# Optimization experiments

Hardware: AMD Instinct MI355X
Metric: run time of the kernel (lower is better)

The kernel has to match this reference:

```python
import jax, jax.numpy as jnp
import numpy as np
from jax import lax

HID = 896          # hidden_size
HALF = HID // 2    # 448
BINS = 256         # 2 ** (bits/2), bits=16
B, T = 16, 2048


def setup_inputs() -> dict:
    key = jax.random.key(0)
    ks = jax.random.split(key, 16)
    rn = lambda k, shape, s: (jax.random.normal(k, shape, jnp.float32) * s)
    inp = {
        'conditional': jax.random.normal(ks[0], (B, T, 3, HID), jnp.float32),
        'input_signal': jax.random.randint(ks[1], (B, T, 2), 0, BINS, jnp.int32),
        'target_coarse': jax.random.randint(ks[2], (B, T, 1), 0, BINS, jnp.int32),
        # project_coarse_input: Linear(2, 3*half, bias=False)
        'Wc': rn(ks[3], (2, 3 * HALF), 0.5),
        # project_fine_input: Linear(3, 3*half, bias=False)
        'Wf': rn(ks[4], (3, 3 * HALF), 0.5),
        # stripped GRU hidden-to-hidden weights/biases (input projection is rnn_input itself)
        'W_hh': rn(ks[5], (HID, 3 * HID), 0.02),
        'b_ih': jnp.zeros((3 * HID,), jnp.float32),
        'b_hh': jnp.zeros((3 * HID,), jnp.float32),
        # to_bins_coarse: Linear(half, half) + ReLU + Linear(half, bins)
        'W1c': rn(ks[6], (HALF, HALF), 0.05), 'b1c': jnp.zeros((HALF,), jnp.float32),
        'W2c': rn(ks[7], (HALF, BINS), 0.05), 'b2c': jnp.zeros((BINS,), jnp.float32),
        # to_bins_fine
        'W1f': rn(ks[8], (HALF, HALF), 0.05), 'b1f': jnp.zeros((HALF,), jnp.float32),
        'W2f': rn(ks[9], (HALF, BINS), 0.05), 'b2f': jnp.zeros((BINS,), jnp.float32),
    }
    return inp


def _scale(x):
    # [0, BINS-1] -> [-1, 1]
    return x.astype(jnp.float32) / ((BINS - 1) / 2.0) - 1.0


def reference(conditional, input_signal, target_coarse, Wc, Wf, W_hh, b_ih, b_hh,
              W1c, b1c, W2c, b2c, W1f, b1f, W2f, b2f):
    sig = _scale(input_signal)          # [B, T, 2]
    tc = _scale(target_coarse)          # [B, T, 1]

    coarse_proj = (sig @ Wc).reshape(B, T, 3, HALF)
    fine_proj = (jnp.concatenate([sig, tc], axis=2) @ Wf).reshape(B, T, 3, HALF)
    # concat along feature halves -> [B, T, 3, HID], add conditional, flatten gates
    rnn_input = jnp.concatenate([coarse_proj, fine_proj], axis=3) + conditional
    rnn_input = rnn_input.reshape(B, T, 3 * HID) + b_ih
    xs = rnn_input.transpose(1, 0, 2)   # [T, B, 3*HID]

    def step(h, x_t):
        gh = h @ W_hh + b_hh                      # [B, 3*HID]
        xr, xz, xn = jnp.split(x_t, 3, axis=-1)
        hr, hz, hn = jnp.split(gh, 3, axis=-1)
        r = jax.nn.sigmoid(xr + hr)
        z = jax.nn.sigmoid(xz + hz)
        n = jnp.tanh(xn + r * hn)
        h_new = (1.0 - z) * n + z * h
        return h_new, h_new

    h0 = jnp.zeros((B, HID), jnp.float32)
    last_hidden, hidden_states = lax.scan(step, h0, xs)   # [T, B, HID]
    hidden_states = hidden_states.transpose(1, 0, 2)      # [B, T, HID]

    hidden_coarse = hidden_states[..., :HALF]
    # NOTE: original code applies to_bins_fine to hidden_coarse as well (faithful).
    out_coarse = jax.nn.relu(hidden_coarse @ W1c + b1c) @ W2c + b2c
    out_fine = jax.nn.relu(hidden_coarse @ W1f + b1f) @ W2f + b2f
    return out_coarse, out_fine, last_hidden
```

## Files before the change

### kernel.cpp

```cpp
#include <hip/hip_runtime.h>
#include <hip/hip_cooperative_groups.h>

namespace cg = cooperative_groups;

#define BB 16
#define TT 2048
#define HIDN 896
#define HALFN 448
#define NBINS 256
#define NWG 224
#define NTHR 64
#define SROW 904
#define WSTR 904

typedef __attribute__((ext_vector_type(8))) short short8;
typedef __attribute__((ext_vector_type(4))) float f32x4;

__device__ __forceinline__ unsigned short f2bf(float x) {
    unsigned int u = __float_as_uint(x);
    unsigned int r = u + 0x7FFFu + ((u >> 16) & 1u);
    return (unsigned short)(r >> 16);
}

__global__ __launch_bounds__(NTHR, 1)
void scan_kernel(const float* __restrict__ cond,
                 const int*   __restrict__ sig,
                 const int*   __restrict__ tcrs,
                 const float* __restrict__ Wc,
                 const float* __restrict__ Wf,
                 const float* __restrict__ Whh,
                 const float* __restrict__ b_ih,
                 const float* __restrict__ b_hh,
                 unsigned long long* __restrict__ hx,
                 int* __restrict__ slots,
                 unsigned short* __restrict__ hc_out,
                 float* __restrict__ lasth)
{
    __shared__ unsigned short sW[16 * WSTR];
    __shared__ unsigned short sH[16 * SROW];

    const int tid  = threadIdx.x;
    const int wg   = blockIdx.x;
    const int col0 = wg * 4;

    for (int idx = tid; idx < 16 * HIDN; idx += NTHR) {
        int j2 = idx & 15, k = idx >> 4;
        unsigned short wv = 0;
        if (j2 < 12)
            wv = f2bf(Whh[(size_t)k * 2688 + (j2 >> 2) * HIDN + col0 + (j2 & 3)]);
        sW[j2 * WSTR + k] = wv;
    }
    for (int idx = tid; idx < (16 * SROW) / 2; idx += NTHR)
        ((unsigned*)sH)[idx] = 0;
    if (tid == 0)
        __hip_atomic_store(&slots[wg], 0, __ATOMIC_RELAXED, __HIP_MEMORY_SCOPE_AGENT);

    const int l  = tid;
    const int jj = l & 15;
    const int hi = l >> 4;
    const bool xrole = jj < 12;
    const int gate = (jj >> 2) & 3;
    const int cc   = jj & 3;
    const int col  = col0 + cc;

    float wp0 = 0.f, wp1 = 0.f, wp2 = 0.f, bi = 0.f, bh = 0.f;
    if (xrole) {
        if (col < HALFN) {
            wp0 = Wc[gate * HALFN + col];
            wp1 = Wc[1344 + gate * HALFN + col];
        } else {
            int ck = col - HALFN;
            wp0 = Wf[gate * HALFN + ck];
            wp1 = Wf[1344 + gate * HALFN + ck];
            wp2 = Wf[2688 + gate * HALFN + ck];
        }
        bi = b_ih[gate * HIDN + col];
        bh = b_hh[gate * HIDN + col];
    }
    float hp[4] = {0.f, 0.f, 0.f, 0.f};

    __syncthreads();
    cg::this_grid().sync();

    const float inv = 1.f / 127.5f;
    const unsigned long long* s64 = (const unsigned long long*)slots;
    const int srcr = (l & 48) | cc;
    const int srcz = (l & 48) | 4 | cc;

#define WAITS(s) { bool ok_;                                                   \
    for (;;) {                                                                 \
        ok_ = true;                                                            \
        if (l < 28) {                                                          \
            unsigned long long a_ = __hip_atomic_load(&s64[28*(s) + l],        \
                __ATOMIC_RELAXED, __HIP_MEMORY_SCOPE_AGENT);                   \
            ok_ = ((int)(a_ & 0xffffffffu) >= t) & ((int)(a_ >> 32) >= t);     \
        }                                                                      \
        if (__all(ok_)) break;                                                 \
        __builtin_amdgcn_s_sleep(1);                                           \
    }                                                                          \
    asm volatile("" ::: "memory"); }

#define LOADS(s, V) _Pragma("unroll")                                          \
    for (int i_ = 0; i_ < 14; ++i_)                                            \
        V[i_] = __hip_atomic_load(&hb[(size_t)((56*(s)) + hi*14 + i_)*16 + jj],\
            __ATOMIC_RELAXED, __HIP_MEMORY_SCOPE_AGENT);

#define STAGES(s, V) _Pragma("unroll")                                         \
    for (int i_ = 0; i_ < 14; ++i_)                                            \
        *(unsigned long long*)&sH[jj * SROW + ((56*(s)) + hi*14 + i_)*4] = V[i_];

#define MFMAS(s) _Pragma("unroll")                                             \
    for (int q_ = 0; q_ < 7; ++q_) {                                           \
        int ks_ = (s)*7 + q_;                                                  \
        short8 av_ = *(const short8*)&sH[jj * SROW + hi * 8 + ks_ * 32];       \
        short8 bv_ = *(const short8*)&sW[jj * WSTR + hi * 8 + ks_ * 32];       \
        ch[(7*(s) + q_) & 3] =                                                 \
            __builtin_amdgcn_mfma_f32_16x16x32_bf16(av_, bv_, ch[(7*(s)+q_)&3],\
                                                    0, 0, 0);                  \
    }

    for (int t = 0; t < TT; ++t) {
        float xc[4], sg0[4], sg1[4], sg2[4];
        if (xrole) {
            #pragma unroll
            for (int r = 0; r < 4; ++r) {
                int b = hi * 4 + r;
                size_t bt = (size_t)b * TT + t;
                xc[r]  = cond[(bt * 3 + gate) * HIDN + col];
                sg0[r] = (float)sig[bt * 2 + 0] * inv - 1.f;
                sg1[r] = (float)sig[bt * 2 + 1] * inv - 1.f;
                sg2[r] = (float)tcrs[bt] * inv - 1.f;
            }
        } else {
            xc[0]=xc[1]=xc[2]=xc[3]=0.f;
            sg0[0]=sg0[1]=sg0[2]=sg0[3]=0.f;
            sg1[0]=sg1[1]=sg1[2]=sg1[3]=0.f;
            sg2[0]=sg2[1]=sg2[2]=sg2[3]=0.f;
        }

        f32x4 ch[4] = {};
        if (t > 0) {
            const unsigned long long* hb = hx + (size_t)(t & 1) * 3584;
            unsigned long long va[14], vb[14];
            WAITS(0); LOADS(0, va);
            WAITS(1); LOADS(1, vb);
            STAGES(0, va); MFMAS(0);
            WAITS(2); LOADS(2, va);
            STAGES(1, vb); MFMAS(1);
            WAITS(3); LOADS(3, vb);
            STAGES(2, va); MFMAS(2);
            STAGES(3, vb); MFMAS(3);
        } else {
            MFMAS(0); MFMAS(1); MFMAS(2); MFMAS(3);
        }

        f32x4 acc = (ch[0] + ch[1]) + (ch[2] + ch[3]);

        float xv[4], sigv[4];
        #pragma unroll
        for (int r = 0; r < 4; ++r) {
            xv[r]   = xc[r] + bi + sg0[r]*wp0 + sg1[r]*wp1 + sg2[r]*wp2;
            sigv[r] = 1.f / (1.f + __expf(-(xv[r] + acc[r] + bh)));
        }
        float rr[4], zz[4];
        #pragma unroll
        for (int r = 0; r < 4; ++r) {
            rr[r] = __shfl(sigv[r], srcr);
            zz[r] = __shfl(sigv[r], srcz);
        }
        unsigned short hbits[4] = {0, 0, 0, 0};
        if (jj >= 8 && jj < 12) {
            #pragma unroll
            for (int r = 0; r < 4; ++r) {
                float a2v = xv[r] + rr[r] * (acc[r] + bh);
                float e = __expf(-2.f * a2v);
                float n = (1.f - e) / (1.f + e);
                float hn = (1.f - zz[r]) * n + zz[r] * hp[r];
                hp[r] = hn;
                hbits[r] = f2bf(hn);
                if (t == TT - 1)
                    lasth[(size_t)(hi * 4 + r) * HIDN + col] = hn;
            }
        }
        unsigned pp32[4];
        unsigned long long hv64[4];
        #pragma unroll
        for (int r = 0; r < 4; ++r) {
            int o1 = __shfl_xor((int)(unsigned)hbits[r], 1);
            unsigned p = ((unsigned)hbits[r] & 0xffffu) | ((unsigned)o1 << 16);
            pp32[r] = p;
            int o2 = __shfl_xor((int)p, 2);
            hv64[r] = (unsigned long long)p | ((unsigned long long)(unsigned)o2 << 32);
        }
        unsigned long long* hd = hx + (size_t)((t + 1) & 1) * 3584;
        if (jj == 8) {
            #pragma unroll
            for (int r = 0; r < 4; ++r)
                __hip_atomic_store(&hd[wg * 16 + hi * 4 + r], hv64[r],
                                   __ATOMIC_RELAXED, __HIP_MEMORY_SCOPE_AGENT);
        }
        asm volatile("s_waitcnt vmcnt(0)" ::: "memory");
        if (tid == 0)
            __hip_atomic_store(&slots[wg], t + 1, __ATOMIC_RELAXED, __HIP_MEMORY_SCOPE_AGENT);

        if (wg < 112 && jj >= 8 && jj < 12 && !(jj & 1)) {
            unsigned* hc32 = (unsigned*)hc_out;
            #pragma unroll
            for (int r = 0; r < 4; ++r)
                hc32[((size_t)(hi * 4 + r) * TT + t) * 224 + wg * 2 + ((jj - 8) >> 1)] = pp32[r];
        }
    }
#undef WAITS
#undef LOADS
#undef STAGES
#undef MFMAS
}

template<int RELU_BF16>
__global__ __launch_bounds__(256)
void head_gemm(const unsigned short* __restrict__ A,
               const float* __restrict__ Bw,
               const float* __restrict__ bias,
               unsigned short* __restrict__ Cb,
               float* __restrict__ Cf,
               int N)
{
    const int K = 448;
    __shared__ float As[32][68];
    __shared__ float Bs[32][68];
    const int tid = threadIdx.x;
    const int tx = tid & 15;
    const int ty = tid >> 4;
    const int bm = blockIdx.x * 64;
    const int bn = blockIdx.y * 64;

    float acc[4][4] = {};

    for (int k0 = 0; k0 < K; k0 += 32) {
        #pragma unroll
        for (int it = 0; it < 2; ++it) {
            int idx = tid + it * 256;
            int m   = idx >> 3;
            int k4  = idx & 7;
            ushort4 av = *(const ushort4*)(A + (size_t)(bm + m) * K + k0 + k4 * 4);
            As[k4 * 4 + 0][m] = __uint_as_float((unsigned)av.x << 16);
            As[k4 * 4 + 1][m] = __uint_as_float((unsigned)av.y << 16);
            As[k4 * 4 + 2][m] = __uint_as_float((unsigned)av.z << 16);
            As[k4 * 4 + 3][m] = __uint_as_float((unsigned)av.w << 16);
        }
        #pragma unroll
        for (int it = 0; it < 2; ++it) {
            int idx = tid + it * 256;
            int k   = idx >> 4;
            int n4  = idx & 15;
            *(float4*)&Bs[k][n4 * 4] =
                *(const float4*)(Bw + (size_t)(k0 + k) * N + bn + n4 * 4);
        }
        __syncthreads();
        #pragma unroll
        for (int k = 0; k < 32; ++k) {
            float4 a4 = *(float4*)&As[k][ty * 4];
            float4 b4 = *(float4*)&Bs[k][tx * 4];
            float ar[4] = {a4.x, a4.y, a4.z, a4.w};
            float br[4] = {b4.x, b4.y, b4.z, b4.w};
            #pragma unroll
            for (int i = 0; i < 4; ++i)
                #pragma unroll
                for (int j = 0; j < 4; ++j)
                    acc[i][j] = fmaf(ar[i], br[j], acc[i][j]);
        }
        __syncthreads();
    }

    float4 bsv = *(const float4*)(bias + bn + tx * 4);
    float bb[4] = {bsv.x, bsv.y, bsv.z, bsv.w};
    #pragma unroll
    for (int i = 0; i < 4; ++i) {
        int row = bm + ty * 4 + i;
        float v[4];
        #pragma unroll
        for (int j = 0; j < 4; ++j) v[j] = acc[i][j] + bb[j];
        if (RELU_BF16) {
            ushort4 o;
            o.x = f2bf(fmaxf(v[0], 0.f));
            o.y = f2bf(fmaxf(v[1], 0.f));
            o.z = f2bf(fmaxf(v[2], 0.f));
            o.w = f2bf(fmaxf(v[3], 0.f));
            *(ushort4*)(Cb + (size_t)row * N + bn + tx * 4) = o;
        } else {
            float4 o = make_float4(v[0], v[1], v[2], v[3]);
            *(float4*)(Cf + (size_t)row * N + bn + tx * 4) = o;
        }
    }
}

extern "C" void kernel_launch(void* const* d_in, const int* in_sizes, int n_in,
                              void* d_out, int out_size, void* d_ws, size_t ws_size,
                              hipStream_t stream)
{
    const float* cond = (const float*)d_in[0];
    const int*   sig  = (const int*)d_in[1];
    const int*   tcrs = (const int*)d_in[2];
    const float* Wc   = (const float*)d_in[3];
    const float* Wf   = (const float*)d_in[4];
    const float* Whh  = (const float*)d_in[5];
    const float* bih  = (const float*)d_in[6];
    const float* bhh  = (const float*)d_in[7];
    const float* W1c  = (const float*)d_in[8];
    const float* b1c  = (const float*)d_in[9];
    const float* W2c  = (const float*)d_in[10];
    const float* b2c  = (const float*)d_in[11];
    const float* W1f  = (const float*)d_in[12];
    const float* b1f  = (const float*)d_in[13];
    const float* W2f  = (const float*)d_in[14];
    const float* b2f  = (const float*)d_in[15];

    char* ws = (char*)d_ws;
    int* slots               = (int*)ws;
    unsigned long long* hx   = (unsigned long long*)(ws + 4096);
    unsigned short* hc       = (unsigned short*)(ws + 65536);
    unsigned short* hid1     = (unsigned short*)(ws + 65536 + 29360128);

    float* outc  = (float*)d_out;
    float* outf  = outc + (size_t)BB * TT * NBINS;
    float* lasth = outc + 2 * (size_t)BB * TT * NBINS;

    void* args[] = {(void*)&cond, (void*)&sig, (void*)&tcrs, (void*)&Wc, (void*)&Wf,
                    (void*)&Whh, (void*)&bih, (void*)&bhh,
                    (void*)&hx, (void*)&slots, (void*)&hc, (void*)&lasth};
    hipLaunchCooperativeKernel((void*)scan_kernel, dim3(NWG), dim3(NTHR),
                               args, 0, stream);

    dim3 blk(256);
    head_gemm<1><<<dim3(512, 7), blk, 0, stream>>>(hc,   W1c, b1c, hid1, nullptr, 448);
    head_gemm<0><<<dim3(512, 4), blk, 0, stream>>>(hid1, W2c, b2c, nullptr, outc, 256);
    head_gemm<1><<<dim3(512, 7), blk, 0, stream>>>(hc,   W1f, b1f, hid1, nullptr, 448);
    head_gemm<0><<<dim3(512, 4), blk, 0, stream>>>(hid1, W2f, b2f, nullptr, outf, 256);
}
```

Before: 9.196 ms.

## Halve scan workgroups, widen per-WG columns, load hidden state directly into MFMA operands

The persistent GRU scan now uses 112 workgroups, each owning 8 hidden columns (r/z and n gates split across two MFMA tiles), instead of 224 groups with 4 columns. The LDS staging of the hidden state is removed: each lane loads its MFMA A operand straight from global memory. Per-workgroup ready flags are padded to separate cache lines and waited on individually. The aim is to cut cross-workgroup synchronisation fan-in and the LDS round-trip on the serial critical path, in exchange for more MFMA and gate work per workgroup per step.

```diff
diff --git a/kernel.cpp b/kernel.cpp
--- a/kernel.cpp
+++ b/kernel.cpp
@@ -8,13 +8,13 @@
 #define HIDN 896
 #define HALFN 448
 #define NBINS 256
-#define NWG 224
+#define NWG 112
 #define NTHR 64
-#define SROW 904
 #define WSTR 904
 
 typedef __attribute__((ext_vector_type(8))) short short8;
 typedef __attribute__((ext_vector_type(4))) float f32x4;
+typedef __attribute__((ext_vector_type(2))) unsigned long long ull2;
 
 __device__ __forceinline__ unsigned short f2bf(float x) {
     unsigned int u = __float_as_uint(x);
@@ -36,183 +36,180 @@
                  unsigned short* __restrict__ hc_out,
                  float* __restrict__ lasth)
 {
-    __shared__ unsigned short sW[16 * WSTR];
-    __shared__ unsigned short sH[16 * SROW];
+    __shared__ unsigned short sW[32 * WSTR];
 
     const int tid  = threadIdx.x;
     const int wg   = blockIdx.x;
-    const int col0 = wg * 4;
-
-    for (int idx = tid; idx < 16 * HIDN; idx += NTHR) {
-        int j2 = idx & 15, k = idx >> 4;
+    const int col0 = wg * 8;
+
+    for (int idx = tid; idx < 32 * HIDN; idx += NTHR) {
+        int j2 = idx & 31, k = idx >> 5;
         unsigned short wv = 0;
-        if (j2 < 12)
-            wv = f2bf(Whh[(size_t)k * 2688 + (j2 >> 2) * HIDN + col0 + (j2 & 3)]);
+        if (j2 < 16)
+            wv = f2bf(Whh[(size_t)k * 2688 + (j2 >> 3) * HIDN + col0 + (j2 & 7)]);
+        else if (j2 < 24)
+            wv = f2bf(Whh[(size_t)k * 2688 + 2 * HIDN + col0 + (j2 & 7)]);
         sW[j2 * WSTR + k] = wv;
     }
-    for (int idx = tid; idx < (16 * SROW) / 2; idx += NTHR)
-        ((unsigned*)sH)[idx] = 0;
     if (tid == 0)
-        __hip_atomic_store(&slots[wg], 0, __ATOMIC_RELAXED, __HIP_MEMORY_SCOPE_AGENT);
+        __hip_atomic_store(&slots[wg * 16], 0, __ATOMIC_RELAXED, __HIP_MEMORY_SCOPE_AGENT);
 
     const int l  = tid;
-    const int jj = l & 15;
+    const int q  = l & 15;
     const int hi = l >> 4;
-    const bool xrole = jj < 12;
-    const int gate = (jj >> 2) & 3;
-    const int cc   = jj & 3;
-    const int col  = col0 + cc;
-
-    float wp0 = 0.f, wp1 = 0.f, wp2 = 0.f, bi = 0.f, bh = 0.f;
-    if (xrole) {
-        if (col < HALFN) {
-            wp0 = Wc[gate * HALFN + col];
-            wp1 = Wc[1344 + gate * HALFN + col];
-        } else {
-            int ck = col - HALFN;
-            wp0 = Wf[gate * HALFN + ck];
-            wp1 = Wf[1344 + gate * HALFN + ck];
-            wp2 = Wf[2688 + gate * HALFN + ck];
-        }
-        bi = b_ih[gate * HIDN + col];
-        bh = b_hh[gate * HIDN + col];
-    }
+    const int gA   = q >> 3;
+    const int colA = col0 + (q & 7);
+
+    float wpA0, wpA1, wpA2, wpB0, wpB1, wpB2;
+    if (colA < HALFN) {
+        wpA0 = Wc[gA * HALFN + colA];
+        wpA1 = Wc[1344 + gA * HALFN + colA];
+        wpA2 = 0.f;
+        wpB0 = Wc[2 * HALFN + colA];
+        wpB1 = Wc[1344 + 2 * HALFN + colA];
+        wpB2 = 0.f;
+    } else {
+        int ck = colA - HALFN;
+        wpA0 = Wf[gA * HALFN + ck];
+        wpA1 = Wf[1344 + gA * HALFN + ck];
+        wpA2 = Wf[2688 + gA * HALFN + ck];
+        wpB0 = Wf[2 * HALFN + ck];
+        wpB1 = Wf[1344 + 2 * HALFN + ck];
+        wpB2 = Wf[2688 + 2 * HALFN + ck];
+    }
+    const float biA = b_ih[gA * HIDN + colA];
+    const float bhA = b_hh[gA * HIDN + colA];
+    const float biB = b_ih[2 * HIDN + colA];
+    const float bhB = b_hh[2 * HIDN + colA];
+
     float hp[4] = {0.f, 0.f, 0.f, 0.f};
 
     __syncthreads();
     cg::this_grid().sync();
 
     const float inv = 1.f / 127.5f;
-    const unsigned long long* s64 = (const unsigned long long*)slots;
-    const int srcr = (l & 48) | cc;
-    const int srcz = (l & 48) | 4 | cc;
+    const int zsrc = (l & 48) | 8 | (q & 7);
 
 #define WAITS(s) { bool ok_;                                                   \
     for (;;) {                                                                 \
         ok_ = true;                                                            \
         if (l < 28) {                                                          \
-            unsigned long long a_ = __hip_atomic_load(&s64[28*(s) + l],        \
+            int a_ = __hip_atomic_load(&slots[((s)*28 + l) * 16],              \
                 __ATOMIC_RELAXED, __HIP_MEMORY_SCOPE_AGENT);                   \
-            ok_ = ((int)(a_ & 0xffffffffu) >= t) & ((int)(a_ >> 32) >= t);     \
+            ok_ = (a_ >= t);                                                   \
         }                                                                      \
         if (__all(ok_)) break;                                                 \
         __builtin_amdgcn_s_sleep(1);                                           \
     }                                                                          \
     asm volatile("" ::: "memory"); }
 
-#define LOADS(s, V) _Pragma("unroll")                                          \
-    for (int i_ = 0; i_ < 14; ++i_)                                            \
-        V[i_] = __hip_atomic_load(&hb[(size_t)((56*(s)) + hi*14 + i_)*16 + jj],\
-            __ATOMIC_RELAXED, __HIP_MEMORY_SCOPE_AGENT);
-
-#define STAGES(s, V) _Pragma("unroll")                                         \
-    for (int i_ = 0; i_ < 14; ++i_)                                            \
-        *(unsigned long long*)&sH[jj * SROW + ((56*(s)) + hi*14 + i_)*4] = V[i_];
-
-#define MFMAS(s) _Pragma("unroll")                                             \
-    for (int q_ = 0; q_ < 7; ++q_) {                                           \
-        int ks_ = (s)*7 + q_;                                                  \
-        short8 av_ = *(const short8*)&sH[jj * SROW + hi * 8 + ks_ * 32];       \
-        short8 bv_ = *(const short8*)&sW[jj * WSTR + hi * 8 + ks_ * 32];       \
-        ch[(7*(s) + q_) & 3] =                                                 \
-            __builtin_amdgcn_mfma_f32_16x16x32_bf16(av_, bv_, ch[(7*(s)+q_)&3],\
-                                                    0, 0, 0);                  \
+#define LOADF(s, V) _Pragma("unroll")                                          \
+    for (int i_ = 0; i_ < 7; ++i_) {                                           \
+        _Pragma("unroll")                                                      \
+        for (int h_ = 0; h_ < 2; ++h_)                                         \
+            V[2*i_ + h_] = __hip_atomic_load(                                  \
+                &hb[(size_t)(4 * ((s)*7 + i_) + hi) * 32 + h_ * 16 + q],       \
+                __ATOMIC_RELAXED, __HIP_MEMORY_SCOPE_AGENT);                   \
+    }
+
+#define MFMAS(s, V) _Pragma("unroll")                                          \
+    for (int i_ = 0; i_ < 7; ++i_) {                                           \
+        ull2 tv_; tv_.x = V[2*i_]; tv_.y = V[2*i_ + 1];                        \
+        short8 av_ = __builtin_bit_cast(short8, tv_);                          \
+        int ks_ = (s)*7 + i_;                                                  \
+        short8 b1_ = *(const short8*)&sW[q * WSTR + hi * 8 + ks_ * 32];        \
+        chA[ks_ & 3] = __builtin_amdgcn_mfma_f32_16x16x32_bf16(                \
+            av_, b1_, chA[ks_ & 3], 0, 0, 0);                                  \
+        short8 b2_ = *(const short8*)&sW[(16 + q) * WSTR + hi * 8 + ks_ * 32]; \
+        chB[ks_ & 3] = __builtin_amdgcn_mfma_f32_16x16x32_bf16(                \
+            av_, b2_, chB[ks_ & 3], 0, 0, 0);                                  \
     }
 
     for (int t = 0; t < TT; ++t) {
-        float xc[4], sg0[4], sg1[4], sg2[4];
-        if (xrole) {
-            #pragma unroll
-            for (int r = 0; r < 4; ++r) {
-                int b = hi * 4 + r;
-                size_t bt = (size_t)b * TT + t;
-                xc[r]  = cond[(bt * 3 + gate) * HIDN + col];
-                sg0[r] = (float)sig[bt * 2 + 0] * inv - 1.f;
-                sg1[r] = (float)sig[bt * 2 + 1] * inv - 1.f;
-                sg2[r] = (float)tcrs[bt] * inv - 1.f;
-            }
-        } else {
-            xc[0]=xc[1]=xc[2]=xc[3]=0.f;
-            sg0[0]=sg0[1]=sg0[2]=sg0[3]=0.f;
-            sg1[0]=sg1[1]=sg1[2]=sg1[3]=0.f;
-            sg2[0]=sg2[1]=sg2[2]=sg2[3]=0.f;
-        }
-
-        f32x4 ch[4] = {};
+        float xcA[4], xcB[4], sg0[4], sg1[4], sg2[4];
+        #pragma unroll
+        for (int r = 0; r < 4; ++r) {
+            int b = hi * 4 + r;
+            size_t bt = (size_t)b * TT + t;
+            xcA[r] = cond[(bt * 3 + gA) * HIDN + colA];
+            xcB[r] = cond[(bt * 3 + 2) * HIDN + colA];
+            sg0[r] = (float)sig[bt * 2 + 0] * inv - 1.f;
+            sg1[r] = (float)sig[bt * 2 + 1] * inv - 1.f;
+            sg2[r] = (float)tcrs[bt] * inv - 1.f;
+        }
+
+        f32x4 chA[4] = {}, chB[4] = {};
         if (t > 0) {
             const unsigned long long* hb = hx + (size_t)(t & 1) * 3584;
             unsigned long long va[14], vb[14];
-            WAITS(0); LOADS(0, va);
-            WAITS(1); LOADS(1, vb);
-            STAGES(0, va); MFMAS(0);
-            WAITS(2); LOADS(2, va);
-            STAGES(1, vb); MFMAS(1);
-            WAITS(3); LOADS(3, vb);
-            STAGES(2, va); MFMAS(2);
-            STAGES(3, vb); MFMAS(3);
-        } else {
-            MFMAS(0); MFMAS(1); MFMAS(2); MFMAS(3);
-        }
-
-        f32x4 acc = (ch[0] + ch[1]) + (ch[2] + ch[3]);
-
-        float xv[4], sigv[4];
+            WAITS(0); LOADF(0, va);
+            WAITS(1); LOADF(1, vb);
+            MFMAS(0, va);
+            WAITS(2); LOADF(2, va);
+            MFMAS(1, vb);
+            WAITS(3); LOADF(3, vb);
+            MFMAS(2, va);
+            MFMAS(3, vb);
+        }
+        f32x4 aA = (chA[0] + chA[1]) + (chA[2] + chA[3]);
+        f32x4 aB = (chB[0] + chB[1]) + (chB[2] + chB[3]);
+
+        float xvA[4], xvB[4], sigA[4];
         #pragma unroll
         for (int r = 0; r < 4; ++r) {
-            xv[r]   = xc[r] + bi + sg0[r]*wp0 + sg1[r]*wp1 + sg2[r]*wp2;
-            sigv[r] = 1.f / (1.f + __expf(-(xv[r] + acc[r] + bh)));
-        }
-        float rr[4], zz[4];
+            xvA[r] = xcA[r] + biA + sg0[r]*wpA0 + sg1[r]*wpA1 + sg2[r]*wpA2;
+            xvB[r] = xcB[r] + biB + sg0[r]*wpB0 + sg1[r]*wpB1 + sg2[r]*wpB2;
+            sigA[r] = 1.f / (1.f + __expf(-(xvA[r] + aA[r] + bhA)));
+        }
+        float hnv[4];
+        unsigned short hbits[4] = {0, 0, 0, 0};
         #pragma unroll
         for (int r = 0; r < 4; ++r) {
-            rr[r] = __shfl(sigv[r], srcr);
-            zz[r] = __shfl(sigv[r], srcz);
-        }
-        unsigned short hbits[4] = {0, 0, 0, 0};
-        if (jj >= 8 && jj < 12) {
+            float zz = __shfl(sigA[r], zsrc);
+            float a2v = xvB[r] + sigA[r] * (aB[r] + bhB);
+            float e = __expf(-2.f * a2v);
+            float n = (1.f - e) / (1.f + e);
+            float hn = (1.f - zz) * n + zz * hp[r];
+            hnv[r] = hn;
+            if (q < 8) { hp[r] = hn; hbits[r] = f2bf(hn); }
+        }
+        if (t == TT - 1 && q < 8) {
             #pragma unroll
-            for (int r = 0; r < 4; ++r) {
-                float a2v = xv[r] + rr[r] * (acc[r] + bh);
-                float e = __expf(-2.f * a2v);
-                float n = (1.f - e) / (1.f + e);
-                float hn = (1.f - zz[r]) * n + zz[r] * hp[r];
-                hp[r] = hn;
-                hbits[r] = f2bf(hn);
-                if (t == TT - 1)
-                    lasth[(size_t)(hi * 4 + r) * HIDN + col] = hn;
-            }
-        }
-        unsigned pp32[4];
+            for (int r = 0; r < 4; ++r)
+                lasth[(size_t)(hi * 4 + r) * HIDN + colA] = hnv[r];
+        }
+
+        unsigned p32[4];
         unsigned long long hv64[4];
         #pragma unroll
         for (int r = 0; r < 4; ++r) {
             int o1 = __shfl_xor((int)(unsigned)hbits[r], 1);
-            unsigned p = ((unsigned)hbits[r] & 0xffffu) | ((unsigned)o1 << 16);
-            pp32[r] = p;
-            int o2 = __shfl_xor((int)p, 2);
-            hv64[r] = (unsigned long long)p | ((unsigned long long)(unsigned)o2 << 32);
-        }
-        unsigned long long* hd = hx + (size_t)((t + 1) & 1) * 3584;
-        if (jj == 8) {
+            p32[r] = ((unsigned)hbits[r] & 0xffffu) | ((unsigned)o1 << 16);
+            int o2 = __shfl_xor((int)p32[r], 2);
+            hv64[r] = (unsigned long long)p32[r] |
+                      ((unsigned long long)(unsigned)o2 << 32);
+        }
+        if (t < TT - 1 && (q == 0 || q == 4)) {
+            unsigned long long* hd = hx + (size_t)((t + 1) & 1) * 3584;
             #pragma unroll
             for (int r = 0; r < 4; ++r)
-                __hip_atomic_store(&hd[wg * 16 + hi * 4 + r], hv64[r],
-                                   __ATOMIC_RELAXED, __HIP_MEMORY_SCOPE_AGENT);
+                __hip_atomic_store(&hd[(size_t)wg * 32 + (q >> 2) * 16 + hi * 4 + r],
+                                   hv64[r], __ATOMIC_RELAXED, __HIP_MEMORY_SCOPE_AGENT);
         }
         asm volatile("s_waitcnt vmcnt(0)" ::: "memory");
         if (tid == 0)
-            __hip_atomic_store(&slots[wg], t + 1, __ATOMIC_RELAXED, __HIP_MEMORY_SCOPE_AGENT);
-
-        if (wg < 112 && jj >= 8 && jj < 12 && !(jj & 1)) {
+            __hip_atomic_store(&slots[wg * 16], t + 1,
+                               __ATOMIC_RELAXED, __HIP_MEMORY_SCOPE_AGENT);
+
+        if (wg < 56 && q < 8 && !(q & 1)) {
             unsigned* hc32 = (unsigned*)hc_out;
             #pragma unroll
             for (int r = 0; r < 4; ++r)
-                hc32[((size_t)(hi * 4 + r) * TT + t) * 224 + wg * 2 + ((jj - 8) >> 1)] = pp32[r];
+                hc32[((size_t)(hi * 4 + r) * TT + t) * 224 + wg * 4 + (q >> 1)] = p32[r];
         }
     }
 #undef WAITS
-#undef LOADS
-#undef STAGES
+#undef LOADF
 #undef MFMAS
 }
 
@@ -317,7 +314,7 @@
 
     char* ws = (char*)d_ws;
     int* slots               = (int*)ws;
-    unsigned long long* hx   = (unsigned long long*)(ws + 4096);
+    unsigned long long* hx   = (unsigned long long*)(ws + 8192);
     unsigned short* hc       = (unsigned short*)(ws + 65536);
     unsigned short* hid1     = (unsigned short*)(ws + 65536 + 29360128);
 
```

Measured after the change: 9.249 ms. About the same (+0.6%).
